# Kernel optimization log

Measured on AMD Instinct MI355X. Metric: run time of the kernel, lower is better.

Reference implementation:

```python
import jax, jax.numpy as jnp
import numpy as np

N = 100000
E = 3200000
IN, HID, OUT = 512, 256, 64
K = 10
ALPHA = 0.1


def setup_inputs() -> dict:
    key = jax.random.key(0)
    ks = jax.random.split(key, 8)
    x = jax.random.normal(ks[0], (N, IN), dtype=jnp.float32)
    edge_index = jax.random.randint(ks[1], (2, E), 0, N, dtype=jnp.int64)
    W1 = jax.random.normal(ks[2], (IN, HID), dtype=jnp.float32) / np.sqrt(IN)
    b1 = jnp.zeros((HID,), dtype=jnp.float32)
    W2 = jax.random.normal(ks[3], (HID, OUT), dtype=jnp.float32) / np.sqrt(HID)
    b2 = jnp.zeros((OUT,), dtype=jnp.float32)
    # PPR init: temp[k] = alpha*(1-alpha)^k, temp[K] = (1-alpha)^K
    temp = ALPHA * (1.0 - ALPHA) ** np.arange(K + 1)
    temp[-1] = (1.0 - ALPHA) ** K
    temp = jnp.asarray(temp, dtype=jnp.float32)
    return {"x": x, "edge_index": edge_index, "W1": W1, "b1": b1,
            "W2": W2, "b2": b2, "temp": temp}


def reference(x, edge_index, W1, b1, W2, b2, temp):
    n = x.shape[0]
    # MLP (dropout = identity in eval mode)
    h = jax.nn.relu(x @ W1 + b1) @ W2 + b2  # [N, OUT]

    # gcn_norm: add self-loops, edge_weight = 1, sym-normalize
    loops = jnp.arange(n, dtype=edge_index.dtype)
    row = jnp.concatenate([edge_index[0], loops])  # source (x_j)
    col = jnp.concatenate([edge_index[1], loops])  # target (aggregate into)
    w = jnp.ones(row.shape[0], dtype=h.dtype)
    deg = jax.ops.segment_sum(w, col, num_segments=n)
    dinv = jnp.where(deg > 0, jax.lax.rsqrt(deg), 0.0)
    norm = dinv[row] * w * dinv[col]  # [E+N]

    hidden = h * temp[0]

    def step(carry, gamma):
        cur, hid = carry
        msg = norm[:, None] * cur[row]                       # gather+scale
        cur = jax.ops.segment_sum(msg, col, num_segments=n)  # scatter-add
        hid = hid + gamma * cur
        return (cur, hid), None

    (_, hidden), _ = jax.lax.scan(step, (h, hidden), temp[1:])
    return hidden
```

## Files before the change

### kernel.cpp

```cpp
#include <hip/hip_runtime.h>
#include <hip/hip_bf16.h>

#define NN   100000
#define EE   3200000
#define INF  512
#define HIDF 256
#define OUTF 64
#define KSTEPS 10

typedef __attribute__((ext_vector_type(8))) short short8;
typedef __attribute__((ext_vector_type(4))) float floatx4;
typedef unsigned short ushort_t;

static __device__ inline short bf2s(__hip_bfloat16 h) {
    return __builtin_bit_cast(short, h);
}

static __device__ inline unsigned short f2bf(float f) {
    unsigned u = __float_as_uint(f);
    unsigned r = (u + 0x7FFFu + ((u >> 16) & 1u)) >> 16;
    return (unsigned short)r;
}

static __device__ inline float b2f(unsigned short u) {
    return __uint_as_float(((unsigned)u) << 16);
}


__global__ void zero_kernel(int* p, int n) {
    int i = blockIdx.x * 256 + threadIdx.x;
    if (i < n) p[i] = 0;
}

__global__ void count_kernel(const int* __restrict__ ei, int* __restrict__ counts) {
    int e = blockIdx.x * 256 + threadIdx.x;
    if (e < EE) atomicAdd(&counts[ei[EE + e]], 1);
}

__global__ void dinv_kernel(const int* __restrict__ counts, float* __restrict__ dinv) {
    int i = blockIdx.x * 256 + threadIdx.x;
    if (i < NN) dinv[i] = rsqrtf((float)(counts[i] + 1));
}

__global__ void scan1(const int* __restrict__ counts, int* __restrict__ offs,
                      int* __restrict__ partial) {
    __shared__ int s[256];
    int tid = threadIdx.x;
    int i = blockIdx.x * 256 + tid;
    int v = (i < NN) ? counts[i] : 0;
    s[tid] = v;
    __syncthreads();
    for (int d = 1; d < 256; d <<= 1) {
        int t = (tid >= d) ? s[tid - d] : 0;
        __syncthreads();
        s[tid] += t;
        __syncthreads();
    }
    if (i < NN) offs[i] = s[tid] - v;
    if (tid == 255) partial[blockIdx.x] = s[255];
}

__global__ void scan2(int* partial, int nblocks) {
    __shared__ int s[512];
    int tid = threadIdx.x;
    int v = (tid < nblocks) ? partial[tid] : 0;
    s[tid] = v;
    __syncthreads();
    for (int d = 1; d < 512; d <<= 1) {
        int t = (tid >= d) ? s[tid - d] : 0;
        __syncthreads();
        s[tid] += t;
        __syncthreads();
    }
    if (tid < nblocks) partial[tid] = s[tid] - v;
}

__global__ void scan3(int* __restrict__ offs, const int* __restrict__ partial) {
    int i = blockIdx.x * 256 + threadIdx.x;
    if (i < NN) offs[i] += partial[i >> 8];
    else if (i == NN) offs[NN] = EE;
}

__global__ void fill_kernel(const int* __restrict__ ei, const int* __restrict__ offs,
                            int* __restrict__ counts, int* __restrict__ srcIdx) {
    int e = blockIdx.x * 256 + threadIdx.x;
    if (e >= EE) return;
    int r = ei[e];
    int c = ei[EE + e];
    int old = atomicSub(&counts[c], 1);
    srcIdx[offs[c] + old - 1] = r;
}

__global__ void pack_w1(const float* __restrict__ W1, short* __restrict__ W1p) {
    int id = blockIdx.x * 256 + threadIdx.x;
    if (id >= INF * HIDF) return;
    int jj = id & 7, l = (id >> 3) & 15, q = (id >> 7) & 3, t = (id >> 9) & 15, kk = id >> 13;
    int k = kk * 32 + q * 8 + jj, n = t * 16 + l;
    W1p[id] = (short)f2bf(W1[k * HIDF + n]);
}

__global__ void pack_w2(const float* __restrict__ W2, short* __restrict__ W2p) {
    int id = blockIdx.x * 256 + threadIdx.x;
    if (id >= HIDF * OUTF) return;
    int jj = id & 7, l = (id >> 3) & 15, q = (id >> 7) & 3, t = (id >> 9) & 3, kk = id >> 11;
    int k = kk * 32 + q * 8 + jj, n = t * 16 + l;
    W2p[id] = (short)f2bf(W2[k * OUTF + n]);
}


__global__ __launch_bounds__(256) void mlp_kernel(
    const float* __restrict__ x, const short* __restrict__ W1p,
    const short* __restrict__ W2p, const float* __restrict__ b1,
    const float* __restrict__ b2, const float* __restrict__ temp,
    const float* __restrict__ dinv,
    ushort_t* __restrict__ z0, float* __restrict__ out) {

    __shared__ __align__(16) short hlds[64][HIDF + 8];

    int tid = threadIdx.x;
    int wave = tid >> 6, lane = tid & 63;
    int l16 = lane & 15, quad = lane >> 4;
    int brow = blockIdx.x * 64;

    const floatx4 zf = {0.f, 0.f, 0.f, 0.f};
    floatx4 acc[4][4];
#pragma unroll
    for (int mi = 0; mi < 4; mi++)
#pragma unroll
        for (int j = 0; j < 4; j++) acc[mi][j] = zf;

    const float* rp[4];
#pragma unroll
    for (int mi = 0; mi < 4; mi++) {
        int row = brow + mi * 16 + l16;
        if (row > NN - 1) row = NN - 1;
        rp[mi] = x + (size_t)row * INF + quad * 8;
    }

    for (int kk = 0; kk < 16; kk++) {
        short8 a[4];
#pragma unroll
        for (int mi = 0; mi < 4; mi++) {
            const float4* ap = reinterpret_cast<const float4*>(rp[mi] + kk * 32);
            float4 f0 = ap[0];
            float4 f1 = ap[1];
            __hip_bfloat162 q0 = __float22bfloat162_rn(make_float2(f0.x, f0.y));
            __hip_bfloat162 q1 = __float22bfloat162_rn(make_float2(f0.z, f0.w));
            __hip_bfloat162 q2 = __float22bfloat162_rn(make_float2(f1.x, f1.y));
            __hip_bfloat162 q3 = __float22bfloat162_rn(make_float2(f1.z, f1.w));
            short8 av;
            av[0] = bf2s(q0.x); av[1] = bf2s(q0.y);
            av[2] = bf2s(q1.x); av[3] = bf2s(q1.y);
            av[4] = bf2s(q2.x); av[5] = bf2s(q2.y);
            av[6] = bf2s(q3.x); av[7] = bf2s(q3.y);
            a[mi] = av;
        }
        short8 b[4];
#pragma unroll
        for (int j = 0; j < 4; j++) {
            int t = wave * 4 + j;
            b[j] = *reinterpret_cast<const short8*>(
                W1p + (((size_t)(kk * 16 + t) * 64 + quad * 16 + l16) << 3));
        }
#pragma unroll
        for (int mi = 0; mi < 4; mi++)
#pragma unroll
            for (int j = 0; j < 4; j++)
                acc[mi][j] = __builtin_amdgcn_mfma_f32_16x16x32_bf16(a[mi], b[j], acc[mi][j], 0, 0, 0);
    }

#pragma unroll
    for (int j = 0; j < 4; j++) {
        float bj = b1[wave * 64 + j * 16 + l16];
#pragma unroll
        for (int mi = 0; mi < 4; mi++)
#pragma unroll
            for (int r = 0; r < 4; r++) {
                float v = acc[mi][j][r] + bj;
                v = fmaxf(v, 0.f);
                hlds[mi * 16 + quad * 4 + r][wave * 64 + j * 16 + l16] = (short)f2bf(v);
            }
    }
    __syncthreads();

    floatx4 acc2[4];
#pragma unroll
    for (int j = 0; j < 4; j++) acc2[j] = zf;

#pragma unroll
    for (int kk = 0; kk < 8; kk++) {
        short8 a2 = *reinterpret_cast<const short8*>(&hlds[wave * 16 + l16][kk * 32 + quad * 8]);
#pragma unroll
        for (int j = 0; j < 4; j++) {
            short8 bb = *reinterpret_cast<const short8*>(
                W2p + (((size_t)(kk * 4 + j) * 64 + quad * 16 + l16) << 3));
            acc2[j] = __builtin_amdgcn_mfma_f32_16x16x32_bf16(a2, bb, acc2[j], 0, 0, 0);
        }
    }

    float t0 = temp[0];
#pragma unroll
    for (int j = 0; j < 4; j++) {
        float bb = b2[j * 16 + l16];
#pragma unroll
        for (int r = 0; r < 4; r++) {
            int row = brow + wave * 16 + quad * 4 + r;
            if (row < NN) {
                float v = acc2[j][r] + bb;
                size_t o = (size_t)row * 64 + j * 16 + l16;
                out[o] = t0 * v;
                z0[o] = f2bf(dinv[row] * v);
            }
        }
    }
}


__global__ __launch_bounds__(256) void prop_kernel(
    const int* __restrict__ srcIdx, const int* __restrict__ offs,
    const float* __restrict__ dinv, const ushort_t* __restrict__ z,
    ushort_t* __restrict__ zn, float* __restrict__ hid,
    const float* __restrict__ temp, int k, int write_z) {

    int node = blockIdx.x * 4 + (threadIdx.x >> 6);
    if (node >= NN) return;
    int f = threadIdx.x & 63;
    int beg = __builtin_amdgcn_readfirstlane(offs[node]);
    int end = __builtin_amdgcn_readfirstlane(offs[node + 1]);
    size_t o = (size_t)node * 64 + f;
    float acc = b2f(z[o]);

    int e = beg;
    for (; e + 4 <= end; e += 4) {
        int s0 = srcIdx[e];
        int s1 = srcIdx[e + 1];
        int s2 = srcIdx[e + 2];
        int s3 = srcIdx[e + 3];
        float v0 = b2f(z[(size_t)s0 * 64 + f]);
        float v1 = b2f(z[(size_t)s1 * 64 + f]);
        float v2 = b2f(z[(size_t)s2 * 64 + f]);
        float v3 = b2f(z[(size_t)s3 * 64 + f]);
        acc += v0 + v1 + v2 + v3;
    }
    for (; e < end; ++e) {
        acc += b2f(z[(size_t)srcIdx[e] * 64 + f]);
    }

    float dv = dinv[node];
    float cn = dv * acc;
    hid[o] += temp[k] * cn;
    if (write_z) zn[o] = f2bf(dv * cn);
}


extern "C" void kernel_launch(void* const* d_in, const int* in_sizes, int n_in,
                              void* d_out, int out_size, void* d_ws, size_t ws_size,
                              hipStream_t stream) {
    const float* x    = (const float*)d_in[0];
    const int*   ei   = (const int*)d_in[1];
    const float* W1   = (const float*)d_in[2];
    const float* b1   = (const float*)d_in[3];
    const float* W2   = (const float*)d_in[4];
    const float* b2   = (const float*)d_in[5];
    const float* temp = (const float*)d_in[6];
    float* out = (float*)d_out;

    char* p = (char*)d_ws;
    auto carve = [&](size_t bytes) -> char* {
        char* r = p;
        p += (bytes + 255) & ~(size_t)255;
        return r;
    };
    ushort_t* zA   = (ushort_t*)carve(sizeof(ushort_t) * (size_t)NN * 64);
    ushort_t* zB   = (ushort_t*)carve(sizeof(ushort_t) * (size_t)NN * 64);
    int* srcIdx    = (int*)carve(sizeof(int) * (size_t)EE);
    int* counts    = (int*)carve(sizeof(int) * NN);
    int* offs      = (int*)carve(sizeof(int) * (NN + 1));
    int* partial   = (int*)carve(sizeof(int) * 512);
    float* dinv    = (float*)carve(sizeof(float) * NN);
    short* W1p     = (short*)carve(sizeof(short) * INF * HIDF);
    short* W2p     = (short*)carve(sizeof(short) * HIDF * OUTF);

    const int NB = (NN + 255) / 256;

    zero_kernel<<<NB, 256, 0, stream>>>(counts, NN);
    pack_w1<<<(INF * HIDF + 255) / 256, 256, 0, stream>>>(W1, W1p);
    pack_w2<<<(HIDF * OUTF + 255) / 256, 256, 0, stream>>>(W2, W2p);

    count_kernel<<<EE / 256, 256, 0, stream>>>(ei, counts);
    dinv_kernel<<<NB, 256, 0, stream>>>(counts, dinv);
    scan1<<<NB, 256, 0, stream>>>(counts, offs, partial);
    scan2<<<1, 512, 0, stream>>>(partial, NB);
    scan3<<<(NN + 256) / 256, 256, 0, stream>>>(offs, partial);
    fill_kernel<<<EE / 256, 256, 0, stream>>>(ei, offs, counts, srcIdx);

    mlp_kernel<<<(NN + 63) / 64, 256, 0, stream>>>(x, W1p, W2p, b1, b2, temp, dinv, zA, out);

    ushort_t* a = zA;
    ushort_t* b = zB;
    for (int k = 1; k <= KSTEPS; k++) {
        prop_kernel<<<NN / 4, 256, 0, stream>>>(srcIdx, offs, dinv, a, b, out, temp, k,
                                                (k < KSTEPS) ? 1 : 0);
        ushort_t* t = a; a = b; b = t;
    }
}
```

Baseline: 1.427 ms.

## Pack bf16 pairs per lane in propagation and vectorize CSR build kernels

The propagation kernel now has each lane load a packed pair of bf16 features as one 32-bit word. The two half-waves each gather a different neighbour row and are combined with a cross-half shuffle, so every wave covers two edges per load instead of one. Neighbour indices are made wave-uniform with readfirstlane, and hid is updated with float2 accesses. The count and fill kernels read four edges per thread through int4 loads, and fill now uses a separate cursor array seeded from the offsets. The aim is to cut gather load instructions and per-edge launch overhead, at the cost of idle half-waves on odd-degree tails and some extra shuffle work.

```diff
diff --git a/kernel.cpp b/kernel.cpp
--- a/kernel.cpp
+++ b/kernel.cpp
@@ -16,14 +16,9 @@
     return __builtin_bit_cast(short, h);
 }
 
-static __device__ inline unsigned short f2bf(float f) {
+static __device__ inline unsigned f2bf(float f) {
     unsigned u = __float_as_uint(f);
-    unsigned r = (u + 0x7FFFu + ((u >> 16) & 1u)) >> 16;
-    return (unsigned short)r;
-}
-
-static __device__ inline float b2f(unsigned short u) {
-    return __uint_as_float(((unsigned)u) << 16);
+    return (u + 0x7FFFu + ((u >> 16) & 1u)) >> 16;
 }
 
 
@@ -33,8 +28,13 @@
 }
 
 __global__ void count_kernel(const int* __restrict__ ei, int* __restrict__ counts) {
-    int e = blockIdx.x * 256 + threadIdx.x;
-    if (e < EE) atomicAdd(&counts[ei[EE + e]], 1);
+    int t = blockIdx.x * 256 + threadIdx.x;
+    if (t >= EE / 4) return;
+    int4 c4 = reinterpret_cast<const int4*>(ei + EE)[t];
+    atomicAdd(&counts[c4.x], 1);
+    atomicAdd(&counts[c4.y], 1);
+    atomicAdd(&counts[c4.z], 1);
+    atomicAdd(&counts[c4.w], 1);
 }
 
 __global__ void dinv_kernel(const int* __restrict__ counts, float* __restrict__ dinv) {
@@ -81,14 +81,25 @@
     else if (i == NN) offs[NN] = EE;
 }
 
-__global__ void fill_kernel(const int* __restrict__ ei, const int* __restrict__ offs,
-                            int* __restrict__ counts, int* __restrict__ srcIdx) {
-    int e = blockIdx.x * 256 + threadIdx.x;
-    if (e >= EE) return;
-    int r = ei[e];
-    int c = ei[EE + e];
-    int old = atomicSub(&counts[c], 1);
-    srcIdx[offs[c] + old - 1] = r;
+__global__ void prefill_kernel(const int* __restrict__ offs, int* __restrict__ cursor) {
+    int i = blockIdx.x * 256 + threadIdx.x;
+    if (i < NN) cursor[i] = offs[i + 1];
+}
+
+__global__ void fill_kernel(const int* __restrict__ ei, int* __restrict__ cursor,
+                            int* __restrict__ srcIdx) {
+    int t = blockIdx.x * 256 + threadIdx.x;
+    if (t >= EE / 4) return;
+    int4 r4 = reinterpret_cast<const int4*>(ei)[t];
+    int4 c4 = reinterpret_cast<const int4*>(ei + EE)[t];
+    int p0 = atomicSub(&cursor[c4.x], 1) - 1;
+    int p1 = atomicSub(&cursor[c4.y], 1) - 1;
+    int p2 = atomicSub(&cursor[c4.z], 1) - 1;
+    int p3 = atomicSub(&cursor[c4.w], 1) - 1;
+    srcIdx[p0] = r4.x;
+    srcIdx[p1] = r4.y;
+    srcIdx[p2] = r4.z;
+    srcIdx[p3] = r4.w;
 }
 
 __global__ void pack_w1(const float* __restrict__ W1, short* __restrict__ W1p) {
@@ -209,7 +220,7 @@
                 float v = acc2[j][r] + bb;
                 size_t o = (size_t)row * 64 + j * 16 + l16;
                 out[o] = t0 * v;
-                z0[o] = f2bf(dinv[row] * v);
+                z0[o] = (ushort_t)f2bf(dinv[row] * v);
             }
         }
     }
@@ -218,38 +229,75 @@
 
 __global__ __launch_bounds__(256) void prop_kernel(
     const int* __restrict__ srcIdx, const int* __restrict__ offs,
-    const float* __restrict__ dinv, const ushort_t* __restrict__ z,
-    ushort_t* __restrict__ zn, float* __restrict__ hid,
+    const float* __restrict__ dinv, const unsigned* __restrict__ zu,
+    unsigned* __restrict__ zn, float* __restrict__ hid,
     const float* __restrict__ temp, int k, int write_z) {
 
     int node = blockIdx.x * 4 + (threadIdx.x >> 6);
-    if (node >= NN) return;
-    int f = threadIdx.x & 63;
+    int lane = threadIdx.x & 63;
+    int li = lane & 31, half = lane >> 5;
+
     int beg = __builtin_amdgcn_readfirstlane(offs[node]);
     int end = __builtin_amdgcn_readfirstlane(offs[node + 1]);
-    size_t o = (size_t)node * 64 + f;
-    float acc = b2f(z[o]);
+
+    float ax = 0.f, ay = 0.f;
+    {
+        unsigned u = zu[(size_t)node * 32 + li];
+        if (half == 0) {
+            ax = __uint_as_float(u << 16);
+            ay = __uint_as_float(u & 0xFFFF0000u);
+        }
+    }
 
     int e = beg;
     for (; e + 4 <= end; e += 4) {
-        int s0 = srcIdx[e];
-        int s1 = srcIdx[e + 1];
-        int s2 = srcIdx[e + 2];
-        int s3 = srcIdx[e + 3];
-        float v0 = b2f(z[(size_t)s0 * 64 + f]);
-        float v1 = b2f(z[(size_t)s1 * 64 + f]);
-        float v2 = b2f(z[(size_t)s2 * 64 + f]);
-        float v3 = b2f(z[(size_t)s3 * 64 + f]);
-        acc += v0 + v1 + v2 + v3;
-    }
-    for (; e < end; ++e) {
-        acc += b2f(z[(size_t)srcIdx[e] * 64 + f]);
-    }
-
-    float dv = dinv[node];
-    float cn = dv * acc;
-    hid[o] += temp[k] * cn;
-    if (write_z) zn[o] = f2bf(dv * cn);
+        int s0 = __builtin_amdgcn_readfirstlane(srcIdx[e]);
+        int s1 = __builtin_amdgcn_readfirstlane(srcIdx[e + 1]);
+        int s2 = __builtin_amdgcn_readfirstlane(srcIdx[e + 2]);
+        int s3 = __builtin_amdgcn_readfirstlane(srcIdx[e + 3]);
+        int sa = half ? s1 : s0;
+        int sb = half ? s3 : s2;
+        unsigned ua = zu[(size_t)sa * 32 + li];
+        unsigned ub = zu[(size_t)sb * 32 + li];
+        ax += __uint_as_float(ua << 16);
+        ay += __uint_as_float(ua & 0xFFFF0000u);
+        ax += __uint_as_float(ub << 16);
+        ay += __uint_as_float(ub & 0xFFFF0000u);
+    }
+    if (e + 2 <= end) {
+        int s0 = __builtin_amdgcn_readfirstlane(srcIdx[e]);
+        int s1 = __builtin_amdgcn_readfirstlane(srcIdx[e + 1]);
+        int sa = half ? s1 : s0;
+        unsigned ua = zu[(size_t)sa * 32 + li];
+        ax += __uint_as_float(ua << 16);
+        ay += __uint_as_float(ua & 0xFFFF0000u);
+        e += 2;
+    }
+    if (e < end) {
+        int s = __builtin_amdgcn_readfirstlane(srcIdx[e]);
+        unsigned u = zu[(size_t)s * 32 + li];
+        if (half == 0) {
+            ax += __uint_as_float(u << 16);
+            ay += __uint_as_float(u & 0xFFFF0000u);
+        }
+    }
+
+    ax += __shfl_xor(ax, 32, 64);
+    ay += __shfl_xor(ay, 32, 64);
+
+    if (half == 0) {
+        float dv = dinv[node];
+        float cx = dv * ax, cy = dv * ay;
+        float g = temp[k];
+        float2* hp = reinterpret_cast<float2*>(hid + (size_t)node * 64 + 2 * li);
+        float2 h = *hp;
+        h.x += g * cx;
+        h.y += g * cy;
+        *hp = h;
+        if (write_z) {
+            zn[(size_t)node * 32 + li] = f2bf(dv * cx) | (f2bf(dv * cy) << 16);
+        }
+    }
 }
 
 
@@ -271,10 +319,11 @@
         p += (bytes + 255) & ~(size_t)255;
         return r;
     };
-    ushort_t* zA   = (ushort_t*)carve(sizeof(ushort_t) * (size_t)NN * 64);
-    ushort_t* zB   = (ushort_t*)carve(sizeof(ushort_t) * (size_t)NN * 64);
+    unsigned* zA   = (unsigned*)carve(sizeof(unsigned) * (size_t)NN * 32);
+    unsigned* zB   = (unsigned*)carve(sizeof(unsigned) * (size_t)NN * 32);
     int* srcIdx    = (int*)carve(sizeof(int) * (size_t)EE);
     int* counts    = (int*)carve(sizeof(int) * NN);
+    int* cursor    = (int*)carve(sizeof(int) * NN);
     int* offs      = (int*)carve(sizeof(int) * (NN + 1));
     int* partial   = (int*)carve(sizeof(int) * 512);
     float* dinv    = (float*)carve(sizeof(float) * NN);
@@ -287,20 +336,22 @@
     pack_w1<<<(INF * HIDF + 255) / 256, 256, 0, stream>>>(W1, W1p);
     pack_w2<<<(HIDF * OUTF + 255) / 256, 256, 0, stream>>>(W2, W2p);
 
-    count_kernel<<<EE / 256, 256, 0, stream>>>(ei, counts);
+    count_kernel<<<EE / 4 / 256, 256, 0, stream>>>(ei, counts);
     dinv_kernel<<<NB, 256, 0, stream>>>(counts, dinv);
     scan1<<<NB, 256, 0, stream>>>(counts, offs, partial);
     scan2<<<1, 512, 0, stream>>>(partial, NB);
     scan3<<<(NN + 256) / 256, 256, 0, stream>>>(offs, partial);
-    fill_kernel<<<EE / 256, 256, 0, stream>>>(ei, offs, counts, srcIdx);
-
-    mlp_kernel<<<(NN + 63) / 64, 256, 0, stream>>>(x, W1p, W2p, b1, b2, temp, dinv, zA, out);
-
-    ushort_t* a = zA;
-    ushort_t* b = zB;
+    prefill_kernel<<<NB, 256, 0, stream>>>(offs, cursor);
+    fill_kernel<<<EE / 4 / 256, 256, 0, stream>>>(ei, cursor, srcIdx);
+
+    mlp_kernel<<<(NN + 63) / 64, 256, 0, stream>>>(x, W1p, W2p, b1, b2, temp, dinv,
+                                                   (ushort_t*)zA, out);
+
+    unsigned* a = zA;
+    unsigned* b = zB;
     for (int k = 1; k <= KSTEPS; k++) {
         prop_kernel<<<NN / 4, 256, 0, stream>>>(srcIdx, offs, dinv, a, b, out, temp, k,
                                                 (k < KSTEPS) ? 1 : 0);
-        ushort_t* t = a; a = b; b = t;
-    }
-}
+        unsigned* t = a; a = b; b = t;
+    }
+}
```

After: 1.571 ms. 1.1x slower.

## Quantize propagated features to int8 with per-node scales and 4-edge-parallel gather

Applied to the files above, without the earlier changes.

Propagation state is stored as packed int8 with a per-node float scale instead of bf16, halving bytes per gathered neighbour row. The prop kernel now splits each wave into four 16-lane groups that each process a different edge, then reduces across groups with shuffles and requantizes the output. A separate quant kernel converts the MLP output, and the CSR fill uses a precomputed cursor array. This trades accuracy (8-bit features per step) and an extra scale gather per edge for lower memory traffic.

```diff
diff --git a/kernel.cpp b/kernel.cpp
--- a/kernel.cpp
+++ b/kernel.cpp
@@ -16,14 +16,17 @@
     return __builtin_bit_cast(short, h);
 }
 
-static __device__ inline unsigned short f2bf(float f) {
+static __device__ inline unsigned f2bf(float f) {
     unsigned u = __float_as_uint(f);
-    unsigned r = (u + 0x7FFFu + ((u >> 16) & 1u)) >> 16;
-    return (unsigned short)r;
-}
-
-static __device__ inline float b2f(unsigned short u) {
-    return __uint_as_float(((unsigned)u) << 16);
+    return (u + 0x7FFFu + ((u >> 16) & 1u)) >> 16;
+}
+
+static __device__ inline float b2f(unsigned u16) {
+    return __uint_as_float(u16 << 16);
+}
+
+static __device__ inline int sb(unsigned u, int byte) {
+    return (int)(signed char)((u >> (byte * 8)) & 0xFFu);
 }
 
 
@@ -81,14 +84,19 @@
     else if (i == NN) offs[NN] = EE;
 }
 
-__global__ void fill_kernel(const int* __restrict__ ei, const int* __restrict__ offs,
-                            int* __restrict__ counts, int* __restrict__ srcIdx) {
+__global__ void prefill_kernel(const int* __restrict__ offs, int* __restrict__ cursor) {
+    int i = blockIdx.x * 256 + threadIdx.x;
+    if (i < NN) cursor[i] = offs[i + 1];
+}
+
+__global__ void fill_kernel(const int* __restrict__ ei, int* __restrict__ cursor,
+                            int* __restrict__ srcIdx) {
     int e = blockIdx.x * 256 + threadIdx.x;
     if (e >= EE) return;
     int r = ei[e];
     int c = ei[EE + e];
-    int old = atomicSub(&counts[c], 1);
-    srcIdx[offs[c] + old - 1] = r;
+    int pos = atomicSub(&cursor[c], 1) - 1;
+    srcIdx[pos] = r;
 }
 
 __global__ void pack_w1(const float* __restrict__ W1, short* __restrict__ W1p) {
@@ -112,8 +120,7 @@
     const float* __restrict__ x, const short* __restrict__ W1p,
     const short* __restrict__ W2p, const float* __restrict__ b1,
     const float* __restrict__ b2, const float* __restrict__ temp,
-    const float* __restrict__ dinv,
-    ushort_t* __restrict__ z0, float* __restrict__ out) {
+    ushort_t* __restrict__ hb, float* __restrict__ out) {
 
     __shared__ __align__(16) short hlds[64][HIDF + 8];
 
@@ -209,47 +216,115 @@
                 float v = acc2[j][r] + bb;
                 size_t o = (size_t)row * 64 + j * 16 + l16;
                 out[o] = t0 * v;
-                z0[o] = f2bf(dinv[row] * v);
+                hb[o] = (ushort_t)f2bf(v);
             }
         }
     }
+}
+
+
+__global__ __launch_bounds__(256) void quant_kernel(
+    const ushort_t* __restrict__ hb, const float* __restrict__ dinv,
+    unsigned* __restrict__ zq, float* __restrict__ zs) {
+
+    int g = blockIdx.x * 256 + threadIdx.x;
+    int node = g >> 4;
+    int l16 = g & 15;
+    if (node >= NN) return;
+
+    const uint2 hh = *reinterpret_cast<const uint2*>(hb + (size_t)node * 64 + l16 * 4);
+    float dv = dinv[node];
+    float v0 = dv * b2f(hh.x & 0xFFFFu);
+    float v1 = dv * b2f(hh.x >> 16);
+    float v2 = dv * b2f(hh.y & 0xFFFFu);
+    float v3 = dv * b2f(hh.y >> 16);
+
+    float m = fmaxf(fmaxf(fabsf(v0), fabsf(v1)), fmaxf(fabsf(v2), fabsf(v3)));
+    m = fmaxf(m, __shfl_xor(m, 1, 64));
+    m = fmaxf(m, __shfl_xor(m, 2, 64));
+    m = fmaxf(m, __shfl_xor(m, 4, 64));
+    m = fmaxf(m, __shfl_xor(m, 8, 64));
+
+    float si = (m > 0.f) ? 127.0f / m : 0.f;
+    if (l16 == 0) zs[node] = m * (1.0f / 127.0f);
+
+    int q0 = (int)rintf(v0 * si);
+    int q1 = (int)rintf(v1 * si);
+    int q2 = (int)rintf(v2 * si);
+    int q3 = (int)rintf(v3 * si);
+    zq[node * 16 + l16] = (unsigned)(q0 & 0xFF) | ((unsigned)(q1 & 0xFF) << 8) |
+                          ((unsigned)(q2 & 0xFF) << 16) | ((unsigned)(q3 & 0xFF) << 24);
 }
 
 
 __global__ __launch_bounds__(256) void prop_kernel(
     const int* __restrict__ srcIdx, const int* __restrict__ offs,
-    const float* __restrict__ dinv, const ushort_t* __restrict__ z,
-    ushort_t* __restrict__ zn, float* __restrict__ hid,
-    const float* __restrict__ temp, int k, int write_z) {
+    const float* __restrict__ dinv,
+    const unsigned* __restrict__ zq, const float* __restrict__ zs,
+    unsigned* __restrict__ zqn, float* __restrict__ zsn,
+    float* __restrict__ hid, const float* __restrict__ temp, int k, int write_z) {
 
     int node = blockIdx.x * 4 + (threadIdx.x >> 6);
-    if (node >= NN) return;
-    int f = threadIdx.x & 63;
+    int lane = threadIdx.x & 63;
+    int l16 = lane & 15, quad = lane >> 4;
+
     int beg = __builtin_amdgcn_readfirstlane(offs[node]);
     int end = __builtin_amdgcn_readfirstlane(offs[node + 1]);
-    size_t o = (size_t)node * 64 + f;
-    float acc = b2f(z[o]);
-
-    int e = beg;
-    for (; e + 4 <= end; e += 4) {
-        int s0 = srcIdx[e];
-        int s1 = srcIdx[e + 1];
-        int s2 = srcIdx[e + 2];
-        int s3 = srcIdx[e + 3];
-        float v0 = b2f(z[(size_t)s0 * 64 + f]);
-        float v1 = b2f(z[(size_t)s1 * 64 + f]);
-        float v2 = b2f(z[(size_t)s2 * 64 + f]);
-        float v3 = b2f(z[(size_t)s3 * 64 + f]);
-        acc += v0 + v1 + v2 + v3;
-    }
-    for (; e < end; ++e) {
-        acc += b2f(z[(size_t)srcIdx[e] * 64 + f]);
-    }
-
-    float dv = dinv[node];
-    float cn = dv * acc;
-    hid[o] += temp[k] * cn;
-    if (write_z) zn[o] = f2bf(dv * cn);
+
+    float a0 = 0.f, a1 = 0.f, a2 = 0.f, a3 = 0.f;
+
+    {
+        unsigned u = zq[node * 16 + l16];
+        float se = (quad == 0) ? zs[node] : 0.f;
+        a0 = fmaf((float)sb(u, 0), se, a0);
+        a1 = fmaf((float)sb(u, 1), se, a1);
+        a2 = fmaf((float)sb(u, 2), se, a2);
+        a3 = fmaf((float)sb(u, 3), se, a3);
+    }
+
+    for (int e = beg; e < end; e += 4) {
+        int idx = e + quad;
+        int cl = min(idx, end - 1);
+        int src = srcIdx[cl];
+        float se = (idx < end) ? zs[src] : 0.f;
+        unsigned u = zq[src * 16 + l16];
+        a0 = fmaf((float)sb(u, 0), se, a0);
+        a1 = fmaf((float)sb(u, 1), se, a1);
+        a2 = fmaf((float)sb(u, 2), se, a2);
+        a3 = fmaf((float)sb(u, 3), se, a3);
+    }
+
+    a0 += __shfl_xor(a0, 16, 64); a0 += __shfl_xor(a0, 32, 64);
+    a1 += __shfl_xor(a1, 16, 64); a1 += __shfl_xor(a1, 32, 64);
+    a2 += __shfl_xor(a2, 16, 64); a2 += __shfl_xor(a2, 32, 64);
+    a3 += __shfl_xor(a3, 16, 64); a3 += __shfl_xor(a3, 32, 64);
+
+    if (quad == 0) {
+        float dv = dinv[node];
+        float c0 = dv * a0, c1 = dv * a1, c2 = dv * a2, c3 = dv * a3;
+        float g = temp[k];
+        float4* hp = reinterpret_cast<float4*>(hid + (size_t)node * 64 + l16 * 4);
+        float4 h = *hp;
+        h.x += g * c0; h.y += g * c1; h.z += g * c2; h.w += g * c3;
+        *hp = h;
+
+        if (write_z) {
+            float z0f = dv * c0, z1f = dv * c1, z2f = dv * c2, z3f = dv * c3;
+            float m = fmaxf(fmaxf(fabsf(z0f), fabsf(z1f)), fmaxf(fabsf(z2f), fabsf(z3f)));
+            m = fmaxf(m, __shfl_xor(m, 1, 64));
+            m = fmaxf(m, __shfl_xor(m, 2, 64));
+            m = fmaxf(m, __shfl_xor(m, 4, 64));
+            m = fmaxf(m, __shfl_xor(m, 8, 64));
+            float si = (m > 0.f) ? 127.0f / m : 0.f;
+            if (l16 == 0) zsn[node] = m * (1.0f / 127.0f);
+            int q0 = (int)rintf(z0f * si);
+            int q1 = (int)rintf(z1f * si);
+            int q2 = (int)rintf(z2f * si);
+            int q3 = (int)rintf(z3f * si);
+            zqn[node * 16 + l16] = (unsigned)(q0 & 0xFF) | ((unsigned)(q1 & 0xFF) << 8) |
+                                   ((unsigned)(q2 & 0xFF) << 16) | ((unsigned)(q3 & 0xFF) << 24);
+        }
+    }
 }
 
 
@@ -271,10 +346,14 @@
         p += (bytes + 255) & ~(size_t)255;
         return r;
     };
-    ushort_t* zA   = (ushort_t*)carve(sizeof(ushort_t) * (size_t)NN * 64);
-    ushort_t* zB   = (ushort_t*)carve(sizeof(ushort_t) * (size_t)NN * 64);
+    unsigned* zqA  = (unsigned*)carve(sizeof(unsigned) * (size_t)NN * 16);
+    unsigned* zqB  = (unsigned*)carve(sizeof(unsigned) * (size_t)NN * 16);
+    float* zsA     = (float*)carve(sizeof(float) * NN);
+    float* zsB     = (float*)carve(sizeof(float) * NN);
+    ushort_t* hb   = (ushort_t*)carve(sizeof(ushort_t) * (size_t)NN * 64);
     int* srcIdx    = (int*)carve(sizeof(int) * (size_t)EE);
     int* counts    = (int*)carve(sizeof(int) * NN);
+    int* cursor    = (int*)carve(sizeof(int) * NN);
     int* offs      = (int*)carve(sizeof(int) * (NN + 1));
     int* partial   = (int*)carve(sizeof(int) * 512);
     float* dinv    = (float*)carve(sizeof(float) * NN);
@@ -292,15 +371,18 @@
     scan1<<<NB, 256, 0, stream>>>(counts, offs, partial);
     scan2<<<1, 512, 0, stream>>>(partial, NB);
     scan3<<<(NN + 256) / 256, 256, 0, stream>>>(offs, partial);
-    fill_kernel<<<EE / 256, 256, 0, stream>>>(ei, offs, counts, srcIdx);
-
-    mlp_kernel<<<(NN + 63) / 64, 256, 0, stream>>>(x, W1p, W2p, b1, b2, temp, dinv, zA, out);
-
-    ushort_t* a = zA;
-    ushort_t* b = zB;
+    prefill_kernel<<<NB, 256, 0, stream>>>(offs, cursor);
+    fill_kernel<<<EE / 256, 256, 0, stream>>>(ei, cursor, srcIdx);
+
+    mlp_kernel<<<(NN + 63) / 64, 256, 0, stream>>>(x, W1p, W2p, b1, b2, temp, hb, out);
+    quant_kernel<<<NN * 16 / 256, 256, 0, stream>>>(hb, dinv, zqA, zsA);
+
+    unsigned* qa = zqA; unsigned* qb = zqB;
+    float* sa = zsA;    float* sb_ = zsB;
     for (int k = 1; k <= KSTEPS; k++) {
-        prop_kernel<<<NN / 4, 256, 0, stream>>>(srcIdx, offs, dinv, a, b, out, temp, k,
-                                                (k < KSTEPS) ? 1 : 0);
-        ushort_t* t = a; a = b; b = t;
-    }
-}
+        prop_kernel<<<NN / 4, 256, 0, stream>>>(srcIdx, offs, dinv, qa, sa, qb, sb_,
+                                                out, temp, k, (k < KSTEPS) ? 1 : 0);
+        unsigned* tq = qa; qa = qb; qb = tq;
+        float* ts = sa; sa = sb_; sb_ = ts;
+    }
+}
```

Result: slower. 2.050 ms (+43.6%).
